# Kernel optimization log

Measured on AMD Instinct MI355X. Metric: run time of the kernel, lower is better.

Reference implementation:

```python
import jax, jax.numpy as jnp
import numpy as np

N_ENTITIES = 200000
N_USERS = 100000
DIM = 64
N_EDGES = 1000000
N_INTER = 1000000
N_REL = 33
N_INTERACTION_TYPES = 8


def segment_softmax(x, seg, num_segments):
    # two-pass numerically stable segment softmax (torch_scatter.scatter_softmax)
    m = jax.ops.segment_max(x, seg, num_segments=num_segments)
    e = jnp.exp(x - m[seg])
    s = jax.ops.segment_sum(e, seg, num_segments=num_segments)
    return e / s[seg]


def setup_inputs() -> dict:
    key = jax.random.key(0)
    ks = jax.random.split(key, 9)
    return {
        "entity_emb": jax.random.normal(ks[0], (N_ENTITIES, DIM), dtype=jnp.float32),
        "user_emb": jax.random.normal(ks[1], (N_USERS, DIM), dtype=jnp.float32),
        "interaction_emb": jax.random.normal(ks[2], (N_INTERACTION_TYPES, DIM), dtype=jnp.float32),
        "relation_emb": jax.random.normal(ks[3], (N_REL, DIM), dtype=jnp.float32),
        "edge_index": jax.random.randint(ks[4], (2, N_EDGES), 0, N_ENTITIES, dtype=jnp.int32),
        "edge_type": jax.random.randint(ks[5], (N_EDGES,), 1, N_REL, dtype=jnp.int32),
        "user_index": jax.random.randint(ks[6], (N_INTER,), 0, N_USERS, dtype=jnp.int32),
        "item_index": jax.random.randint(ks[7], (N_INTER,), 0, N_ENTITIES, dtype=jnp.int32),
        "interact_type": jax.random.randint(ks[8], (N_INTER,), 0, N_INTERACTION_TYPES, dtype=jnp.int32),
    }


def reference(entity_emb, user_emb, interaction_emb, relation_emb,
              edge_index, edge_type, user_index, item_index, interact_type):
    n_entities = entity_emb.shape[0]
    n_users = user_emb.shape[0]
    head, tail = edge_index[0], edge_index[1]

    # --- entity aggregation over KG edges ---
    neigh = entity_emb[tail]                                      # [E, D]
    w1 = jnp.sum(neigh * relation_emb[edge_type - 1], axis=1) / 8.0   # [E]
    w1 = segment_softmax(w1, head, n_entities)[:, None]           # [E, 1]
    entity_agg = jax.ops.segment_sum(neigh * w1, head, num_segments=n_entities)  # [n_entities, D]

    # --- user aggregation over interactions (agg_method='attention') ---
    interact_entity_emb = entity_emb[item_index]                  # [I, D]
    att = jnp.sum(interaction_emb[interact_type] * user_emb[user_index] * interact_entity_emb, axis=1)  # [I]
    att_w = segment_softmax(att, user_index, n_users)[:, None]    # [I, 1]
    user_agg = jax.ops.segment_sum(att_w * interact_entity_emb, user_index, num_segments=n_users)  # [n_users, D]

    return entity_agg, user_agg, att_w, w1
```

## Files before the change

### kernel.cpp

```cpp
#include <hip/hip_runtime.h>
#include <hip/hip_bf16.h>

#define DIM 64
#define RELS 32
#define SCAN_B 512
#define TILE_V 64

__device__ __forceinline__ unsigned int pk_bf2(float a, float b) {
    unsigned int ua = __float_as_uint(a);
    unsigned int ub = __float_as_uint(b);
    ua = (ua + 0x7fffu + ((ua >> 16) & 1u)) >> 16;
    ub = (ub + 0x7fffu + ((ub >> 16) & 1u)) >> 16;
    return ua | (ub << 16);
}
__device__ __forceinline__ float4 bf4_to_f4(uint2 u) {
    float4 r;
    r.x = __uint_as_float(u.x << 16);
    r.y = __uint_as_float(u.x & 0xffff0000u);
    r.z = __uint_as_float(u.y << 16);
    r.w = __uint_as_float(u.y & 0xffff0000u);
    return r;
}

__global__ __launch_bounds__(256, 4) void buildM_deg(
    const float* __restrict__ ent, const float* __restrict__ rel,
    __hip_bfloat16* __restrict__ M, uint2* __restrict__ entB2,
    const int* __restrict__ head, const int* __restrict__ uidx,
    unsigned int* __restrict__ degP,
    unsigned char* __restrict__ rank_e, unsigned char* __restrict__ rank_i,
    int nE, int E, int I, int gM) {
    __shared__ float4 entL[TILE_V * 17];
    __shared__ float relS[4][16][33];
    int tx = threadIdx.x;
    int bid = blockIdx.x;

    if (bid >= gM) {
        int t = (bid - gM) * 256 + tx;
        if (t < E) {
            int s = head[t];
            unsigned int old = atomicAdd(&degP[s >> 2], 1u << (8 * (s & 3)));
            rank_e[t] = (unsigned char)((old >> (8 * (s & 3))) & 0xFFu);
        } else if (t < E + I) {
            int e = t - E;
            int s = nE + uidx[e];
            unsigned int old = atomicAdd(&degP[s >> 2], 1u << (8 * (s & 3)));
            rank_i[e] = (unsigned char)((old >> (8 * (s & 3))) & 0xFFu);
        }
        return;
    }

    int vg = tx >> 4, rg = tx & 15;
    int base = bid * TILE_V;
    const float4* rel4 = (const float4*)rel;
    #pragma unroll
    for (int k = 0; k < 2; k++) {
        int idx = tx + k * 256;
        float4 v = rel4[idx];
        int r = idx >> 4, d4 = idx & 15;
        relS[0][d4][r] = v.x; relS[1][d4][r] = v.y;
        relS[2][d4][r] = v.z; relS[3][d4][r] = v.w;
    }
    const float4* ent4 = (const float4*)ent;
    #pragma unroll
    for (int k = 0; k < 4; k++) {
        int idx = tx + k * 256;
        int row = idx >> 4, col = idx & 15;
        int v = base + row;
        float4 val = make_float4(0.f, 0.f, 0.f, 0.f);
        if (v < nE) {
            val = ent4[(size_t)v * 16 + col];
            entB2[(size_t)v * 16 + col] = make_uint2(pk_bf2(val.x, val.y), pk_bf2(val.z, val.w));
        }
        entL[row * 17 + col] = val;
    }
    __syncthreads();

    float acc[4][2] = {{0.f,0.f},{0.f,0.f},{0.f,0.f},{0.f,0.f}};
    int r0 = rg * 2;
    #pragma unroll 2
    for (int d4 = 0; d4 < 16; d4++) {
        float4 a0 = entL[(vg * 4 + 0) * 17 + d4];
        float4 a1 = entL[(vg * 4 + 1) * 17 + d4];
        float4 a2 = entL[(vg * 4 + 2) * 17 + d4];
        float4 a3 = entL[(vg * 4 + 3) * 17 + d4];
        float bx0 = relS[0][d4][r0],     by0 = relS[1][d4][r0];
        float bz0 = relS[2][d4][r0],     bw0 = relS[3][d4][r0];
        float bx1 = relS[0][d4][r0 + 1], by1 = relS[1][d4][r0 + 1];
        float bz1 = relS[2][d4][r0 + 1], bw1 = relS[3][d4][r0 + 1];
        acc[0][0] = fmaf(a0.x,bx0, fmaf(a0.y,by0, fmaf(a0.z,bz0, fmaf(a0.w,bw0, acc[0][0]))));
        acc[1][0] = fmaf(a1.x,bx0, fmaf(a1.y,by0, fmaf(a1.z,bz0, fmaf(a1.w,bw0, acc[1][0]))));
        acc[2][0] = fmaf(a2.x,bx0, fmaf(a2.y,by0, fmaf(a2.z,bz0, fmaf(a2.w,bw0, acc[2][0]))));
        acc[3][0] = fmaf(a3.x,bx0, fmaf(a3.y,by0, fmaf(a3.z,bz0, fmaf(a3.w,bw0, acc[3][0]))));
        acc[0][1] = fmaf(a0.x,bx1, fmaf(a0.y,by1, fmaf(a0.z,bz1, fmaf(a0.w,bw1, acc[0][1]))));
        acc[1][1] = fmaf(a1.x,bx1, fmaf(a1.y,by1, fmaf(a1.z,bz1, fmaf(a1.w,bw1, acc[1][1]))));
        acc[2][1] = fmaf(a2.x,bx1, fmaf(a2.y,by1, fmaf(a2.z,bz1, fmaf(a2.w,bw1, acc[2][1]))));
        acc[3][1] = fmaf(a3.x,bx1, fmaf(a3.y,by1, fmaf(a3.z,bz1, fmaf(a3.w,bw1, acc[3][1]))));
    }
    __hip_bfloat162* M2 = (__hip_bfloat162*)M;
    #pragma unroll
    for (int i = 0; i < 4; i++) {
        int v = base + vg * 4 + i;
        if (v < nE) {
            __hip_bfloat16 h0 = __float2bfloat16(acc[i][0] * 0.125f);
            __hip_bfloat16 h1 = __float2bfloat16(acc[i][1] * 0.125f);
            M2[(size_t)v * 16 + rg] = __halves2bfloat162(h0, h1);
        }
    }
}

__global__ __launch_bounds__(SCAN_B) void scan_partial(
    const unsigned int* __restrict__ degP, unsigned int* __restrict__ part, int nW) {
    __shared__ unsigned int lds[SCAN_B];
    int i = blockIdx.x * SCAN_B + threadIdx.x;
    unsigned int v = (i < nW) ? degP[i] : 0u;
    lds[threadIdx.x] = (v & 0xFFu) + ((v >> 8) & 0xFFu) + ((v >> 16) & 0xFFu) + (v >> 24);
    __syncthreads();
    for (int off = SCAN_B >> 1; off > 0; off >>= 1) {
        if (threadIdx.x < off) lds[threadIdx.x] += lds[threadIdx.x + off];
        __syncthreads();
    }
    if (threadIdx.x == 0) part[blockIdx.x] = lds[0];
}

__global__ __launch_bounds__(1024) void scan_block(unsigned int* __restrict__ part, int nb) {
    __shared__ unsigned int lds[1024];
    int t = threadIdx.x;
    unsigned int v = (t < nb) ? part[t] : 0u;
    lds[t] = v;
    __syncthreads();
    for (int off = 1; off < 1024; off <<= 1) {
        unsigned int x = (t >= off) ? lds[t - off] : 0u;
        __syncthreads();
        lds[t] += x;
        __syncthreads();
    }
    if (t < nb) part[t] = lds[t] - v;
}

__global__ __launch_bounds__(SCAN_B) void scan_final(
    const unsigned int* __restrict__ degP, const unsigned int* __restrict__ part,
    unsigned int* __restrict__ offs, int nW) {
    __shared__ unsigned int lds[SCAN_B];
    int t = threadIdx.x;
    int i = blockIdx.x * SCAN_B + t;
    unsigned int v = (i < nW) ? degP[i] : 0u;
    unsigned int b0 = v & 0xFFu, b1 = (v >> 8) & 0xFFu, b2 = (v >> 16) & 0xFFu, b3 = v >> 24;
    unsigned int tot = b0 + b1 + b2 + b3;
    lds[t] = tot;
    __syncthreads();
    for (int off = 1; off < SCAN_B; off <<= 1) {
        unsigned int x = (t >= off) ? lds[t - off] : 0u;
        __syncthreads();
        lds[t] += x;
        __syncthreads();
    }
    if (i < nW) {
        unsigned int base = part[blockIdx.x] + lds[t] - tot;
        uint4 o;
        o.x = base; o.y = base + b0; o.z = base + b0 + b1; o.w = base + b0 + b1 + b2;
        ((uint4*)offs)[i] = o;
    }
}

__global__ __launch_bounds__(256) void scatter32(
    const __hip_bfloat16* __restrict__ M,
    const int* __restrict__ head, const int* __restrict__ tail, const int* __restrict__ etype,
    const int* __restrict__ uidx, const int* __restrict__ iidx, const int* __restrict__ ttype,
    const unsigned char* __restrict__ rank_e, const unsigned char* __restrict__ rank_i,
    const unsigned int* __restrict__ offs,
    unsigned long long* __restrict__ pay64, unsigned int* __restrict__ payu,
    float* __restrict__ e_sc, int E, int I, int nE) {
    int t = blockIdx.x * blockDim.x + threadIdx.x;
    if (t < E) {
        int tl = tail[t];
        float sc = __bfloat162float(M[(size_t)tl * RELS + (etype[t] - 1)]);
        e_sc[t] = sc;
        unsigned int p = offs[head[t]] + rank_e[t];
        unsigned long long v = ((unsigned long long)__float_as_uint(sc) << 32) | (unsigned int)tl;
        __builtin_nontemporal_store(v, &pay64[p]);
    } else if (t < E + I) {
        int e = t - E;
        unsigned int p = offs[nE + uidx[e]] + rank_i[e] - (unsigned)E;
        unsigned int v = (unsigned int)iidx[e] | ((unsigned int)ttype[e] << 27);
        __builtin_nontemporal_store(v, &payu[p]);
    }
}

__global__ __launch_bounds__(256) void fused_agg(
    const uint2* __restrict__ entB2, const float* __restrict__ ent,
    const float* __restrict__ usr, const float* __restrict__ itc,
    const unsigned long long* __restrict__ pay64, const unsigned int* __restrict__ payu,
    const unsigned int* __restrict__ degP, const unsigned int* __restrict__ offs,
    float* __restrict__ patt, float2* __restrict__ msum,
    float* __restrict__ aggE, float* __restrict__ aggU,
    int nE, int nU, int E, int gAE) {
    __shared__ float4 itcL[8][16];
    int tx = threadIdx.x;
    int bid = blockIdx.x;

    if (bid < gAE) {
        int t = bid * 256 + tx;
        int h = t >> 4, l = t & 15;
        if (h >= nE) return;
        unsigned int d = (degP[h >> 2] >> (8 * (h & 3))) & 0xFFu;
        float m = -3.0e38f, s = 0.f, inv = 0.f;
        float4 acc = make_float4(0.f, 0.f, 0.f, 0.f);
        if (d) {
            unsigned int off = offs[h];
            unsigned long long v0 = pay64[off];
            uint2 b0 = entB2[(size_t)(unsigned int)(v0 & 0xffffffffu) * 16 + l];
            for (unsigned int j = 0; j < d; j++) {
                unsigned long long v1 = v0; uint2 b1 = b0;
                if (j + 1 < d) {
                    v1 = pay64[off + j + 1];
                    b1 = entB2[(size_t)(unsigned int)(v1 & 0xffffffffu) * 16 + l];
                }
                float sc = __uint_as_float((unsigned int)(v0 >> 32));
                float4 a0 = bf4_to_f4(b0);
                float mn = fmaxf(m, sc);
                float scale = __expf(m - mn);
                float w = __expf(sc - mn);
                s = s * scale + w;
                acc.x = acc.x * scale + w * a0.x;
                acc.y = acc.y * scale + w * a0.y;
                acc.z = acc.z * scale + w * a0.z;
                acc.w = acc.w * scale + w * a0.w;
                m = mn; v0 = v1; b0 = b1;
            }
            inv = 1.f / s;
        }
        if (l == 0) msum[h] = make_float2(m, inv);
        acc.x *= inv; acc.y *= inv; acc.z *= inv; acc.w *= inv;
        ((float4*)(aggE + (size_t)h * DIM))[l] = acc;
        return;
    }

    if (tx < 128) itcL[tx >> 4][tx & 15] = ((const float4*)itc)[tx];
    __syncthreads();
    int t = (bid - gAE) * 256 + tx;
    int h = t >> 4, l = t & 15;
    if (h >= nU) return;
    int hs = nE + h;
    unsigned int d = (degP[hs >> 2] >> (8 * (hs & 3))) & 0xFFu;
    float m = -3.0e38f, s = 0.f, inv = 0.f;
    float4 acc = make_float4(0.f, 0.f, 0.f, 0.f);
    float4 ur = ((const float4*)(usr + (size_t)h * DIM))[l];
    if (d) {
        unsigned int off = offs[hs] - (unsigned)E;
        unsigned int v0 = payu[off];
        float4 a0 = ((const float4*)(ent + (size_t)(v0 & 0x7ffffffu) * DIM))[l];
        for (unsigned int j = 0; j < d; j++) {
            unsigned int v1 = v0; float4 a1 = a0;
            if (j + 1 < d) {
                v1 = payu[off + j + 1];
                a1 = ((const float4*)(ent + (size_t)(v1 & 0x7ffffffu) * DIM))[l];
            }
            float4 c = itcL[v0 >> 27][l];
            float p = a0.x * ur.x * c.x + a0.y * ur.y * c.y
                    + a0.z * ur.z * c.z + a0.w * ur.w * c.w;
            p += __shfl_xor(p, 1);
            p += __shfl_xor(p, 2);
            p += __shfl_xor(p, 4);
            p += __shfl_xor(p, 8);
            if (l == 0) patt[off + j] = p;
            float mn = fmaxf(m, p);
            float scale = __expf(m - mn);
            float w = __expf(p - mn);
            s = s * scale + w;
            acc.x = acc.x * scale + w * a0.x;
            acc.y = acc.y * scale + w * a0.y;
            acc.z = acc.z * scale + w * a0.z;
            acc.w = acc.w * scale + w * a0.w;
            m = mn; v0 = v1; a0 = a1;
        }
        inv = 1.f / s;
    }
    if (l == 0) msum[hs] = make_float2(m, inv);
    acc.x *= inv; acc.y *= inv; acc.z *= inv; acc.w *= inv;
    ((float4*)(aggU + (size_t)h * DIM))[l] = acc;
}

__global__ __launch_bounds__(256) void wout(
    const int* __restrict__ head, const int* __restrict__ uidx,
    const float* __restrict__ e_sc, const float* __restrict__ patt,
    const unsigned char* __restrict__ rank_i,
    const unsigned int* __restrict__ offs, const float2* __restrict__ msum,
    float* __restrict__ w1, float* __restrict__ attw, int E, int I, int nE) {
    int t = blockIdx.x * blockDim.x + threadIdx.x;
    if (t < E) {
        float2 mi = msum[head[t]];
        w1[t] = __expf(e_sc[t] - mi.x) * mi.y;
    } else if (t < E + I) {
        int e = t - E; int u = uidx[e];
        float2 mi = msum[nE + u];
        float sc = patt[offs[nE + u] - (unsigned)E + rank_i[e]];
        attw[e] = __expf(sc - mi.x) * mi.y;
    }
}

extern "C" void kernel_launch(void* const* d_in, const int* in_sizes, int n_in,
                              void* d_out, int out_size, void* d_ws, size_t ws_size,
                              hipStream_t stream) {
    const float* ent  = (const float*)d_in[0];
    const float* usr  = (const float*)d_in[1];
    const float* itc  = (const float*)d_in[2];
    const float* rel  = (const float*)d_in[3];
    const int* eidx   = (const int*)d_in[4];
    const int* etype  = (const int*)d_in[5];
    const int* uidx   = (const int*)d_in[6];
    const int* iidx   = (const int*)d_in[7];
    const int* ttype  = (const int*)d_in[8];

    const int E  = in_sizes[4] / 2;
    const int I  = in_sizes[6];
    const int nE = in_sizes[0] / DIM;
    const int nU = in_sizes[1] / DIM;
    const int* head = eidx;
    const int* tail = eidx + E;
    const int NSEG = nE + nU;
    const int NW = (NSEG + 3) / 4;
    const int NWpad = (NW + 3) & ~3;
    const int NB = (NW + SCAN_B - 1) / SCAN_B;

    float* out_entity = (float*)d_out;
    float* out_user   = out_entity + (size_t)nE * DIM;
    float* out_attw   = out_user + (size_t)nU * DIM;
    float* out_w1     = out_attw + I;

    unsigned int* degP      = (unsigned int*)d_ws;
    unsigned int* offs      = degP + NWpad;
    unsigned int* part      = offs + NSEG;
    unsigned long long* pay64 = (unsigned long long*)(part + 1024);
    unsigned int* payu      = (unsigned int*)(pay64 + E);
    float* e_sc             = (float*)(payu + I);
    __hip_bfloat16* M       = (__hip_bfloat16*)(e_sc + E);
    uint2* entB2            = (uint2*)(M + (size_t)nE * RELS);
    float2* msum            = (float2*)(entB2 + (size_t)nE * 16);
    float* patt             = (float*)(msum + NSEG);
    unsigned char* rank_e   = (unsigned char*)(patt + I);
    unsigned char* rank_i   = rank_e + E;

    hipMemsetAsync(degP, 0, (size_t)NWpad * sizeof(unsigned int), stream);

    const int T = 256;
    const int gM  = (nE + TILE_V - 1) / TILE_V;
    const int gD  = (E + I + T - 1) / T;
    const int gAE = (int)(((size_t)nE * 16 + T - 1) / T);
    const int gAU = (int)(((size_t)nU * 16 + T - 1) / T);

    buildM_deg<<<dim3((unsigned)(gM + gD)), T, 0, stream>>>(
        ent, rel, M, entB2, head, uidx, degP, rank_e, rank_i, nE, E, I, gM);

    scan_partial<<<dim3((unsigned)NB), SCAN_B, 0, stream>>>(degP, part, NW);
    scan_block<<<dim3(1), 1024, 0, stream>>>(part, NB);
    scan_final<<<dim3((unsigned)NB), SCAN_B, 0, stream>>>(degP, part, offs, NW);

    scatter32<<<dim3((unsigned)gD), T, 0, stream>>>(
        M, head, tail, etype, uidx, iidx, ttype, rank_e, rank_i, offs,
        pay64, payu, e_sc, E, I, nE);

    fused_agg<<<dim3((unsigned)(gAE + gAU)), T, 0, stream>>>(
        entB2, ent, usr, itc, pay64, payu, degP, offs, patt, msum,
        out_entity, out_user, nE, nU, E, gAE);

    wout<<<dim3((unsigned)gD), T, 0, stream>>>(
        head, uidx, e_sc, patt, rank_i, offs, msum, out_w1, out_attw, E, I, nE);
}
```

Measured before the change: 312.9 us.

## Use fp16 entity copy for both aggregations, unpack degree counters, interleave buildM blocks

The packed bf16 entity copy becomes fp16, and the user-attention aggregation now gathers from that half-precision copy instead of the fp32 entity table, halving its gather traffic. Degree counters go from four 8-bit counts packed per word to one 32-bit counter per segment, which removes atomic contention across neighbouring segments and simplifies the scans. The buildM grid interleaves two matrix-build blocks with five degree-count blocks per group of seven so the compute and atomic work overlap. The trade-offs are a larger degree array and the precision limits of fp16 (range and rounding) on the gathered embeddings.

```diff
diff --git a/kernel.cpp b/kernel.cpp
--- a/kernel.cpp
+++ b/kernel.cpp
@@ -1,56 +1,52 @@
 #include <hip/hip_runtime.h>
 #include <hip/hip_bf16.h>
+#include <hip/hip_fp16.h>
 
 #define DIM 64
 #define RELS 32
 #define SCAN_B 512
 #define TILE_V 64
 
-__device__ __forceinline__ unsigned int pk_bf2(float a, float b) {
-    unsigned int ua = __float_as_uint(a);
-    unsigned int ub = __float_as_uint(b);
-    ua = (ua + 0x7fffu + ((ua >> 16) & 1u)) >> 16;
-    ub = (ub + 0x7fffu + ((ub >> 16) & 1u)) >> 16;
-    return ua | (ub << 16);
-}
-__device__ __forceinline__ float4 bf4_to_f4(uint2 u) {
-    float4 r;
-    r.x = __uint_as_float(u.x << 16);
-    r.y = __uint_as_float(u.x & 0xffff0000u);
-    r.z = __uint_as_float(u.y << 16);
-    r.w = __uint_as_float(u.y & 0xffff0000u);
-    return r;
+__device__ __forceinline__ unsigned int pk_h2(float a, float b) {
+    __half2 h = __float22half2_rn(make_float2(a, b));
+    return *reinterpret_cast<unsigned int*>(&h);
+}
+__device__ __forceinline__ float4 h4_to_f4(uint2 u) {
+    __half2 h0 = *reinterpret_cast<__half2*>(&u.x);
+    __half2 h1 = *reinterpret_cast<__half2*>(&u.y);
+    float2 f0 = __half22float2(h0);
+    float2 f1 = __half22float2(h1);
+    return make_float4(f0.x, f0.y, f1.x, f1.y);
 }
 
 __global__ __launch_bounds__(256, 4) void buildM_deg(
     const float* __restrict__ ent, const float* __restrict__ rel,
-    __hip_bfloat16* __restrict__ M, uint2* __restrict__ entB2,
+    __hip_bfloat16* __restrict__ M, uint2* __restrict__ entH,
     const int* __restrict__ head, const int* __restrict__ uidx,
-    unsigned int* __restrict__ degP,
+    unsigned int* __restrict__ deg,
     unsigned char* __restrict__ rank_e, unsigned char* __restrict__ rank_i,
     int nE, int E, int I, int gM) {
     __shared__ float4 entL[TILE_V * 17];
     __shared__ float relS[4][16][33];
     int tx = threadIdx.x;
     int bid = blockIdx.x;
-
-    if (bid >= gM) {
-        int t = (bid - gM) * 256 + tx;
+    int g = bid / 7, slot = bid - g * 7;
+
+    if (slot >= 2) {
+        int t = (g * 5 + (slot - 2)) * 256 + tx;
         if (t < E) {
-            int s = head[t];
-            unsigned int old = atomicAdd(&degP[s >> 2], 1u << (8 * (s & 3)));
-            rank_e[t] = (unsigned char)((old >> (8 * (s & 3))) & 0xFFu);
+            rank_e[t] = (unsigned char)atomicAdd(&deg[head[t]], 1u);
         } else if (t < E + I) {
             int e = t - E;
-            int s = nE + uidx[e];
-            unsigned int old = atomicAdd(&degP[s >> 2], 1u << (8 * (s & 3)));
-            rank_i[e] = (unsigned char)((old >> (8 * (s & 3))) & 0xFFu);
+            rank_i[e] = (unsigned char)atomicAdd(&deg[nE + uidx[e]], 1u);
         }
         return;
     }
 
+    int mb = g * 2 + slot;
+    if (mb >= gM) return;
     int vg = tx >> 4, rg = tx & 15;
-    int base = bid * TILE_V;
+    int base = mb * TILE_V;
     const float4* rel4 = (const float4*)rel;
     #pragma unroll
     for (int k = 0; k < 2; k++) {
@@ -69,7 +65,7 @@
         float4 val = make_float4(0.f, 0.f, 0.f, 0.f);
         if (v < nE) {
             val = ent4[(size_t)v * 16 + col];
-            entB2[(size_t)v * 16 + col] = make_uint2(pk_bf2(val.x, val.y), pk_bf2(val.z, val.w));
+            entH[(size_t)v * 16 + col] = make_uint2(pk_h2(val.x, val.y), pk_h2(val.z, val.w));
         }
         entL[row * 17 + col] = val;
     }
@@ -109,11 +105,10 @@
 }
 
 __global__ __launch_bounds__(SCAN_B) void scan_partial(
-    const unsigned int* __restrict__ degP, unsigned int* __restrict__ part, int nW) {
+    const unsigned int* __restrict__ deg, unsigned int* __restrict__ part, int n) {
     __shared__ unsigned int lds[SCAN_B];
     int i = blockIdx.x * SCAN_B + threadIdx.x;
-    unsigned int v = (i < nW) ? degP[i] : 0u;
-    lds[threadIdx.x] = (v & 0xFFu) + ((v >> 8) & 0xFFu) + ((v >> 16) & 0xFFu) + (v >> 24);
+    lds[threadIdx.x] = (i < n) ? deg[i] : 0u;
     __syncthreads();
     for (int off = SCAN_B >> 1; off > 0; off >>= 1) {
         if (threadIdx.x < off) lds[threadIdx.x] += lds[threadIdx.x + off];
@@ -138,15 +133,13 @@
 }
 
 __global__ __launch_bounds__(SCAN_B) void scan_final(
-    const unsigned int* __restrict__ degP, const unsigned int* __restrict__ part,
-    unsigned int* __restrict__ offs, int nW) {
+    const unsigned int* __restrict__ deg, const unsigned int* __restrict__ part,
+    unsigned int* __restrict__ offs, int n) {
     __shared__ unsigned int lds[SCAN_B];
     int t = threadIdx.x;
     int i = blockIdx.x * SCAN_B + t;
-    unsigned int v = (i < nW) ? degP[i] : 0u;
-    unsigned int b0 = v & 0xFFu, b1 = (v >> 8) & 0xFFu, b2 = (v >> 16) & 0xFFu, b3 = v >> 24;
-    unsigned int tot = b0 + b1 + b2 + b3;
-    lds[t] = tot;
+    unsigned int v = (i < n) ? deg[i] : 0u;
+    lds[t] = v;
     __syncthreads();
     for (int off = 1; off < SCAN_B; off <<= 1) {
         unsigned int x = (t >= off) ? lds[t - off] : 0u;
@@ -154,12 +147,7 @@
         lds[t] += x;
         __syncthreads();
     }
-    if (i < nW) {
-        unsigned int base = part[blockIdx.x] + lds[t] - tot;
-        uint4 o;
-        o.x = base; o.y = base + b0; o.z = base + b0 + b1; o.w = base + b0 + b1 + b2;
-        ((uint4*)offs)[i] = o;
-    }
+    if (i < n) offs[i] = part[blockIdx.x] + lds[t] - v;
 }
 
 __global__ __launch_bounds__(256) void scatter32(
@@ -187,10 +175,10 @@
 }
 
 __global__ __launch_bounds__(256) void fused_agg(
-    const uint2* __restrict__ entB2, const float* __restrict__ ent,
-    const float* __restrict__ usr, const float* __restrict__ itc,
+    const uint2* __restrict__ entH, const float* __restrict__ usr,
+    const float* __restrict__ itc,
     const unsigned long long* __restrict__ pay64, const unsigned int* __restrict__ payu,
-    const unsigned int* __restrict__ degP, const unsigned int* __restrict__ offs,
+    const unsigned int* __restrict__ deg, const unsigned int* __restrict__ offs,
     float* __restrict__ patt, float2* __restrict__ msum,
     float* __restrict__ aggE, float* __restrict__ aggU,
     int nE, int nU, int E, int gAE) {
@@ -202,21 +190,21 @@
         int t = bid * 256 + tx;
         int h = t >> 4, l = t & 15;
         if (h >= nE) return;
-        unsigned int d = (degP[h >> 2] >> (8 * (h & 3))) & 0xFFu;
+        unsigned int d = deg[h];
         float m = -3.0e38f, s = 0.f, inv = 0.f;
         float4 acc = make_float4(0.f, 0.f, 0.f, 0.f);
         if (d) {
             unsigned int off = offs[h];
             unsigned long long v0 = pay64[off];
-            uint2 b0 = entB2[(size_t)(unsigned int)(v0 & 0xffffffffu) * 16 + l];
+            uint2 b0 = entH[(size_t)(unsigned int)(v0 & 0xffffffffu) * 16 + l];
             for (unsigned int j = 0; j < d; j++) {
                 unsigned long long v1 = v0; uint2 b1 = b0;
                 if (j + 1 < d) {
                     v1 = pay64[off + j + 1];
-                    b1 = entB2[(size_t)(unsigned int)(v1 & 0xffffffffu) * 16 + l];
+                    b1 = entH[(size_t)(unsigned int)(v1 & 0xffffffffu) * 16 + l];
                 }
                 float sc = __uint_as_float((unsigned int)(v0 >> 32));
-                float4 a0 = bf4_to_f4(b0);
+                float4 a0 = h4_to_f4(b0);
                 float mn = fmaxf(m, sc);
                 float scale = __expf(m - mn);
                 float w = __expf(sc - mn);
@@ -241,20 +229,21 @@
     int h = t >> 4, l = t & 15;
     if (h >= nU) return;
     int hs = nE + h;
-    unsigned int d = (degP[hs >> 2] >> (8 * (hs & 3))) & 0xFFu;
+    unsigned int d = deg[hs];
     float m = -3.0e38f, s = 0.f, inv = 0.f;
     float4 acc = make_float4(0.f, 0.f, 0.f, 0.f);
     float4 ur = ((const float4*)(usr + (size_t)h * DIM))[l];
     if (d) {
         unsigned int off = offs[hs] - (unsigned)E;
         unsigned int v0 = payu[off];
-        float4 a0 = ((const float4*)(ent + (size_t)(v0 & 0x7ffffffu) * DIM))[l];
+        uint2 b0 = entH[(size_t)(v0 & 0x7ffffffu) * 16 + l];
         for (unsigned int j = 0; j < d; j++) {
-            unsigned int v1 = v0; float4 a1 = a0;
+            unsigned int v1 = v0; uint2 b1 = b0;
             if (j + 1 < d) {
                 v1 = payu[off + j + 1];
-                a1 = ((const float4*)(ent + (size_t)(v1 & 0x7ffffffu) * DIM))[l];
+                b1 = entH[(size_t)(v1 & 0x7ffffffu) * 16 + l];
             }
+            float4 a0 = h4_to_f4(b0);
             float4 c = itcL[v0 >> 27][l];
             float p = a0.x * ur.x * c.x + a0.y * ur.y * c.y
                     + a0.z * ur.z * c.z + a0.w * ur.w * c.w;
@@ -271,7 +260,7 @@
             acc.y = acc.y * scale + w * a0.y;
             acc.z = acc.z * scale + w * a0.z;
             acc.w = acc.w * scale + w * a0.w;
-            m = mn; v0 = v1; a0 = a1;
+            m = mn; v0 = v1; b0 = b1;
         }
         inv = 1.f / s;
     }
@@ -318,49 +307,48 @@
     const int* head = eidx;
     const int* tail = eidx + E;
     const int NSEG = nE + nU;
-    const int NW = (NSEG + 3) / 4;
-    const int NWpad = (NW + 3) & ~3;
-    const int NB = (NW + SCAN_B - 1) / SCAN_B;
+    const int NB = (NSEG + SCAN_B - 1) / SCAN_B;
 
     float* out_entity = (float*)d_out;
     float* out_user   = out_entity + (size_t)nE * DIM;
     float* out_attw   = out_user + (size_t)nU * DIM;
     float* out_w1     = out_attw + I;
 
-    unsigned int* degP      = (unsigned int*)d_ws;
-    unsigned int* offs      = degP + NWpad;
+    unsigned int* deg       = (unsigned int*)d_ws;
+    unsigned int* offs      = deg + NSEG;
     unsigned int* part      = offs + NSEG;
     unsigned long long* pay64 = (unsigned long long*)(part + 1024);
     unsigned int* payu      = (unsigned int*)(pay64 + E);
     float* e_sc             = (float*)(payu + I);
     __hip_bfloat16* M       = (__hip_bfloat16*)(e_sc + E);
-    uint2* entB2            = (uint2*)(M + (size_t)nE * RELS);
-    float2* msum            = (float2*)(entB2 + (size_t)nE * 16);
+    uint2* entH             = (uint2*)(M + (size_t)nE * RELS);
+    float2* msum            = (float2*)(entH + (size_t)nE * 16);
     float* patt             = (float*)(msum + NSEG);
     unsigned char* rank_e   = (unsigned char*)(patt + I);
     unsigned char* rank_i   = rank_e + E;
 
-    hipMemsetAsync(degP, 0, (size_t)NWpad * sizeof(unsigned int), stream);
+    hipMemsetAsync(deg, 0, (size_t)NSEG * sizeof(unsigned int), stream);
 
     const int T = 256;
     const int gM  = (nE + TILE_V - 1) / TILE_V;
     const int gD  = (E + I + T - 1) / T;
+    const int NG  = ((gM + 1) / 2 > (gD + 4) / 5) ? (gM + 1) / 2 : (gD + 4) / 5;
     const int gAE = (int)(((size_t)nE * 16 + T - 1) / T);
     const int gAU = (int)(((size_t)nU * 16 + T - 1) / T);
 
-    buildM_deg<<<dim3((unsigned)(gM + gD)), T, 0, stream>>>(
-        ent, rel, M, entB2, head, uidx, degP, rank_e, rank_i, nE, E, I, gM);
-
-    scan_partial<<<dim3((unsigned)NB), SCAN_B, 0, stream>>>(degP, part, NW);
+    buildM_deg<<<dim3((unsigned)(NG * 7)), T, 0, stream>>>(
+        ent, rel, M, entH, head, uidx, deg, rank_e, rank_i, nE, E, I, gM);
+
+    scan_partial<<<dim3((unsigned)NB), SCAN_B, 0, stream>>>(deg, part, NSEG);
     scan_block<<<dim3(1), 1024, 0, stream>>>(part, NB);
-    scan_final<<<dim3((unsigned)NB), SCAN_B, 0, stream>>>(degP, part, offs, NW);
+    scan_final<<<dim3((unsigned)NB), SCAN_B, 0, stream>>>(deg, part, offs, NSEG);
 
     scatter32<<<dim3((unsigned)gD), T, 0, stream>>>(
         M, head, tail, etype, uidx, iidx, ttype, rank_e, rank_i, offs,
         pay64, payu, e_sc, E, I, nE);
 
     fused_agg<<<dim3((unsigned)(gAE + gAU)), T, 0, stream>>>(
-        entB2, ent, usr, itc, pay64, payu, degP, offs, patt, msum,
+        entH, usr, itc, pay64, payu, deg, offs, patt, msum,
         out_entity, out_user, nE, nU, E, gAE);
 
     wout<<<dim3((unsigned)gD), T, 0, stream>>>(
```

Result: faster. 291.6 us (median of 2 runs) (-6.8%).
